# Kernel tuning notes

Measured on AMD Instinct MI355X. Metric: run time of the kernel, lower is better.

The kernel has to match this reference:

```python
import jax, jax.numpy as jnp
import numpy as np
from jax import lax

N_QUANTIZE = 256
N_AUX = 28
N_RESCH = 512
N_SKIPCH = 256
KS = 2
DILATIONS = [2 ** i for i in range(10)] * 3  # 30 layers
L = len(DILATIONS)


def _causal_conv(x, w, b, d):
    # x: (B, Cin, T), w: (Cout, Cin, KS) torch Conv1d layout, left-pad => causal
    pad = (w.shape[-1] - 1) * d
    y = lax.conv_general_dilated(x, w, window_strides=(1,), padding=[(pad, 0)],
                                 rhs_dilation=(d,),
                                 dimension_numbers=('NCH', 'OIH', 'NCH'))
    return y + b[None, :, None]


def _conv1x1(x, w, b):
    # x: (B, Cin, T), w: (Cout, Cin)
    return jnp.einsum('oi,bit->bot', w, x) + b[None, :, None]


def setup_inputs() -> dict:
    key = jax.random.key(0)
    ks = jax.random.split(key, 20)
    B, T = 2, 8000
    s = 0.05
    rn = lambda k, shape: (jax.random.normal(k, shape, jnp.float32) * s)
    inp = {
        'x': jax.random.randint(ks[0], (B, T), 0, N_QUANTIZE),
        'h': jax.random.normal(ks[1], (B, N_AUX, T), jnp.float32),
        'causal_w': rn(ks[2], (N_RESCH, N_QUANTIZE, KS)),
        'causal_b': rn(ks[3], (N_RESCH,)),
        'dil_sig_w': rn(ks[4], (L, N_RESCH, N_RESCH, KS)),
        'dil_sig_b': rn(ks[5], (L, N_RESCH)),
        'dil_tanh_w': rn(ks[6], (L, N_RESCH, N_RESCH, KS)),
        'dil_tanh_b': rn(ks[7], (L, N_RESCH)),
        'aux_sig_w': rn(ks[8], (L, N_RESCH, N_AUX)),
        'aux_sig_b': rn(ks[9], (L, N_RESCH)),
        'aux_tanh_w': rn(ks[10], (L, N_RESCH, N_AUX)),
        'aux_tanh_b': rn(ks[11], (L, N_RESCH)),
        'skip_w': rn(ks[12], (L, N_SKIPCH, N_RESCH)),
        'skip_b': rn(ks[13], (L, N_SKIPCH)),
        'res_w': rn(ks[14], (L, N_RESCH, N_RESCH)),
        'res_b': rn(ks[15], (L, N_RESCH)),
        'post1_w': rn(ks[16], (N_SKIPCH, N_SKIPCH)),
        'post1_b': rn(ks[17], (N_SKIPCH,)),
        'post2_w': rn(ks[18], (N_QUANTIZE, N_SKIPCH)),
        'post2_b': rn(ks[19], (N_QUANTIZE,)),
    }
    return inp


def reference(x, h, causal_w, causal_b, dil_sig_w, dil_sig_b, dil_tanh_w, dil_tanh_b,
              aux_sig_w, aux_sig_b, aux_tanh_w, aux_tanh_b, skip_w, skip_b,
              res_w, res_b, post1_w, post1_b, post2_w, post2_b):
    B, T = x.shape
    # _preprocess: onehot (B,T,Q) -> (B,Q,T), then causal conv
    oh = jax.nn.one_hot(x % N_QUANTIZE, N_QUANTIZE, dtype=jnp.float32).transpose(0, 2, 1)
    out = _causal_conv(oh, causal_w, causal_b, 1)  # (B, n_resch, T)
    skip_sum = jnp.zeros((B, N_SKIPCH, T), jnp.float32)
    for l, d in enumerate(DILATIONS):
        sig = _causal_conv(out, dil_sig_w[l], dil_sig_b[l], d) + _conv1x1(h, aux_sig_w[l], aux_sig_b[l])
        tan = _causal_conv(out, dil_tanh_w[l], dil_tanh_b[l], d) + _conv1x1(h, aux_tanh_w[l], aux_tanh_b[l])
        z = jax.nn.sigmoid(sig) * jnp.tanh(tan)
        skip_sum = skip_sum + _conv1x1(z, skip_w[l], skip_b[l])
        out = _conv1x1(z, res_w[l], res_b[l]) + out
    # _postprocess: relu -> 1x1 -> relu -> 1x1 -> (B, T, n_quantize)
    y = jax.nn.relu(skip_sum)
    y = jax.nn.relu(_conv1x1(y, post1_w, post1_b))
    y = _conv1x1(y, post2_w, post2_b)
    return y.transpose(0, 2, 1)
```

## Files before the change

### kernel.cpp

```cpp
#include <hip/hip_runtime.h>
#include <math.h>

#define T_LEN 8000
#define BATCH 2
#define CCH 512
#define SKP 256
#define AUXP 32
#define NQ 256
#define NLAYER 30
#define PADF 512
#define TPAD 8192
#define ROWS (PADF + TPAD)
#define HROWS TPAD

typedef unsigned short hfu;
typedef unsigned int u32;
typedef __attribute__((ext_vector_type(8))) _Float16 half8;
typedef __attribute__((ext_vector_type(4))) float f32x4;

#define GLOAD16(g, l)                                                          \
  __builtin_amdgcn_global_load_lds(                                            \
      (const __attribute__((address_space(1))) void*)(g),                      \
      (__attribute__((address_space(3))) void*)(l), 16, 0, 0)

__device__ inline hfu hfbits(float f) {
  union { _Float16 h; hfu u; } x;
  x.h = (_Float16)f;
  return x.u;
}
__device__ inline u32 pk2(float a, float b) {
  return (u32)hfbits(a) | ((u32)hfbits(b) << 16);
}
__device__ inline uint4 pk8(const float f[8]) {
  return make_uint4(pk2(f[0], f[1]), pk2(f[2], f[3]), pk2(f[4], f[5]), pk2(f[6], f[7]));
}
__device__ inline int ldsL(int row, int ck) {
  return ((row >> 1) << 3) + ((((ck) ^ ((row >> 1) & 3)) << 1) | (row & 1));
}

__global__ __launch_bounds__(256) void zero16(uint4* p, int n) {
  for (int i = blockIdx.x * 256 + threadIdx.x; i < n; i += gridDim.x * 256)
    p[i] = make_uint4(0u, 0u, 0u, 0u);
}

__global__ __launch_bounds__(256) void cvt_dil2(const float* __restrict__ inS,
                                                const float* __restrict__ inT,
                                                hfu* __restrict__ outS, hfu* __restrict__ outT) {
  const long NG = (long)NLAYER * CCH * (CCH / 4);
  for (long g2 = (long)blockIdx.x * 256 + threadIdx.x; g2 < 2 * NG; g2 += (long)gridDim.x * 256) {
    const int sel = (int)(g2 >= NG);
    const long g = sel ? (g2 - NG) : g2;
    const float* in = sel ? inT : inS;
    hfu* out = sel ? outT : outS;
    const int i4 = (int)(g & 127) * 4;
    const int o = (int)((g >> 7) & 511);
    const int l = (int)(g >> 16);
    const float* pp = in + (((size_t)l * CCH + o) * CCH + i4) * 2;
    float4 f0 = *(const float4*)pp;
    float4 f1 = *(const float4*)(pp + 4);
    uint2 t0 = make_uint2(pk2(f0.x, f0.z), pk2(f1.x, f1.z));
    uint2 t1 = make_uint2(pk2(f0.y, f0.w), pk2(f1.y, f1.w));
    hfu* ob = out + ((size_t)l * 2 * CCH + o) * CCH + i4;
    *(uint2*)ob = t0;
    *(uint2*)(ob + (size_t)CCH * CCH) = t1;
  }
}

__global__ __launch_bounds__(256) void cvt_skipres(const float* __restrict__ skw,
                                                   const float* __restrict__ rsw,
                                                   hfu* __restrict__ out) {
  const long NG = (long)NLAYER * 768 * (CCH / 4);
  for (long g = (long)blockIdx.x * 256 + threadIdx.x; g < NG; g += (long)gridDim.x * 256) {
    const int i4 = (int)(g & 127) * 4;
    const int r = (int)((g >> 7) % 768);
    const int l = (int)(g / (128 * 768));
    const float* src = (r < SKP) ? (skw + ((size_t)l * SKP + r) * CCH + i4)
                                 : (rsw + ((size_t)l * CCH + (r - SKP)) * CCH + i4);
    float4 f = *(const float4*)src;
    *(uint2*)(out + ((size_t)l * 768 + r) * CCH + i4) = make_uint2(pk2(f.x, f.y), pk2(f.z, f.w));
  }
}

__global__ __launch_bounds__(256) void cvt_aux(const float* __restrict__ in, hfu* __restrict__ out) {
  const int N = NLAYER * CCH * AUXP;
  for (int i = blockIdx.x * 256 + threadIdx.x; i < N; i += gridDim.x * 256) {
    const int j = i & 31;
    const int o = (i >> 5) & 511;
    const int l = i >> 14;
    float v = (j < 28) ? in[((size_t)l * CCH + o) * 28 + j] : 0.f;
    out[i] = hfbits(v);
  }
}

__global__ __launch_bounds__(256) void cvt_copy(const float* __restrict__ in, hfu* __restrict__ out, int n) {
  for (int i = blockIdx.x * 256 + threadIdx.x; i < n; i += gridDim.x * 256)
    out[i] = hfbits(in[i]);
}

__global__ __launch_bounds__(256) void cvt_cwt(const float* __restrict__ cw, float* __restrict__ out) {
  const int N = 2 * NQ * CCH;
  for (int i = blockIdx.x * 256 + threadIdx.x; i < N; i += gridDim.x * 256) {
    const int tap = i >> 17;
    const int r = i & 131071;
    const int xq = r >> 9;
    const int o = r & 511;
    out[i] = cw[((size_t)o * NQ + xq) * 2 + tap];
  }
}

__global__ __launch_bounds__(256) void htrans_kernel(const float* __restrict__ h, hfu* __restrict__ hbf) {
  const int b = blockIdx.y;
  const int t = blockIdx.x * 64 + (threadIdx.x & 63);
  const int j0 = threadIdx.x >> 6;
#pragma unroll
  for (int j = j0; j < AUXP; j += 4) {
    float v = (j < 28 && t < T_LEN) ? h[((size_t)b * 28 + j) * T_LEN + t] : 0.f;
    hbf[((size_t)b * HROWS + t) * AUXP + j] = hfbits(v);
  }
}

template <int PRE>
__global__ __launch_bounds__(256) void embed_kernel(const int* __restrict__ x,
                                                    const float* __restrict__ cwt,
                                                    const float* __restrict__ cb,
                                                    float* __restrict__ outf,
                                                    hfu* __restrict__ outb) {
  const int b = blockIdx.y;
  const int t = blockIdx.x * 4 + (threadIdx.x >> 6);
  const int o = (threadIdx.x & 63) * 8;
  const int xc = x[(size_t)b * T_LEN + t] & 255;
  const int xp = (t > 0) ? (x[(size_t)b * T_LEN + t - 1] & 255) : 0;
  const float won = (t > 0) ? 1.f : 0.f;
  const float* c1 = cwt + 131072 + (size_t)xc * CCH + o;
  const float* c0 = cwt + (size_t)xp * CCH + o;
  float v[8];
#pragma unroll
  for (int j = 0; j < 8; ++j) v[j] = cb[o + j] + c1[j] + won * c0[j];
  if (PRE) {
    *(uint4*)&outb[((size_t)b * ROWS + PADF + t) * CCH + o] = pk8(v);
  } else {
    float* po = outf + ((size_t)b * ROWS + PADF + t) * CCH + o;
    *(float4*)po = make_float4(v[0], v[1], v[2], v[3]);
    *(float4*)(po + 4) = make_float4(v[4], v[5], v[6], v[7]);
  }
}

template <int PRE>
__global__ __launch_bounds__(512, 2) void gate_kernel(
    const hfu* __restrict__ actb, const float* __restrict__ actf,
    const hfu* __restrict__ hbf,
    const void* __restrict__ wsp, const void* __restrict__ wtp,
    const hfu* __restrict__ auxs, const hfu* __restrict__ auxt,
    const float* __restrict__ bs1, const float* __restrict__ bs2,
    const float* __restrict__ bt1, const float* __restrict__ bt2,
    hfu* __restrict__ z, int d) {
  extern __shared__ uint4 smd[];
  const int tid = threadIdx.x;
  const int lane = tid & 63, wid = tid >> 6;
  const int wm = wid >> 2, wn = wid & 3;
  const int lr = lane & 15, lq = lane >> 4;

  const int n = blockIdx.x;
  const int f = (n & 7) * 32 + (n >> 3);
  const int tt = f >> 3, inner = f & 7;
  const int o0 = (inner >> 1) * 128;
  const int b = inner & 1;
  const int t0 = tt * 256;

  f32x4 accS[4][4] = {};
  f32x4 accT[4][4] = {};

  auto stage_dil = [&](int ih, int p) {
    const int base = p * 4096;
    const int tau = (ih < 8) ? 1 : 0;
    const int koff = (ih & 7) * 64;
    if (PRE) {
#pragma unroll
      for (int c = 0; c < 2; ++c) {
        const int s = c * 512 + tid;
        const int row = s >> 3, ck = (s & 7) ^ (row & 7);
        const size_t wo = ((size_t)tau * CCH + o0 + row) * CCH + koff + ck * 8;
        GLOAD16((const hfu*)wsp + wo, &smd[base + s]);
        GLOAD16((const hfu*)wtp + wo, &smd[base + 1024 + s]);
      }
#pragma unroll
      for (int c = 0; c < 4; ++c) {
        const int s = c * 512 + tid;
        const int row = s >> 3, ck = (s & 7) ^ (row & 7);
        const hfu* ar = actb + ((size_t)b * ROWS + PADF + t0 + row - (tau ? 0 : d)) * CCH + koff + ck * 8;
        GLOAD16(ar, &smd[base + 2048 + s]);
      }
    } else {
      const float* wsf = (const float*)wsp;
      const float* wtf = (const float*)wtp;
#pragma unroll
      for (int c = 0; c < 2; ++c) {
        const int s = c * 512 + tid;
        const int row = s >> 3, ck = (s & 7) ^ (row & 7);
        const size_t fb = ((size_t)(o0 + row) * CCH + koff + ck * 8) * 2;
        float vs[8], vt[8];
#pragma unroll
        for (int j = 0; j < 4; ++j) {
          float4 fs = *(const float4*)&wsf[fb + j * 4];
          float4 ft = *(const float4*)&wtf[fb + j * 4];
          vs[2 * j] = tau ? fs.y : fs.x;
          vs[2 * j + 1] = tau ? fs.w : fs.z;
          vt[2 * j] = tau ? ft.y : ft.x;
          vt[2 * j + 1] = tau ? ft.w : ft.z;
        }
        smd[base + s] = pk8(vs);
        smd[base + 1024 + s] = pk8(vt);
      }
#pragma unroll
      for (int c = 0; c < 4; ++c) {
        const int s = c * 512 + tid;
        const int row = s >> 3, ck = (s & 7) ^ (row & 7);
        const float* ar = actf + ((size_t)b * ROWS + PADF + t0 + row - (tau ? 0 : d)) * CCH + koff + ck * 8;
        float4 f0 = *(const float4*)&ar[0];
        float4 f1 = *(const float4*)&ar[4];
        float vb[8] = {f0.x, f0.y, f0.z, f0.w, f1.x, f1.y, f1.z, f1.w};
        smd[base + 2048 + s] = pk8(vb);
      }
    }
  };

  auto stage_aux = [&](int p) {
    const int base = p * 4096;
    {
      const int row = tid >> 2, ck = (tid & 3) ^ (row & 3);
      if (PRE) {
        GLOAD16(auxs + (size_t)(o0 + row) * AUXP + ck * 8, &smd[base + tid]);
        GLOAD16(auxt + (size_t)(o0 + row) * AUXP + ck * 8, &smd[base + 1024 + tid]);
      } else {
        smd[base + tid] = *(const uint4*)&auxs[(size_t)(o0 + row) * AUXP + ck * 8];
        smd[base + 1024 + tid] = *(const uint4*)&auxt[(size_t)(o0 + row) * AUXP + ck * 8];
      }
    }
#pragma unroll
    for (int c = 0; c < 2; ++c) {
      const int s = c * 512 + tid;
      const int row = s >> 2, ck = (s & 3) ^ (row & 3);
      if (PRE)
        GLOAD16(hbf + ((size_t)b * HROWS + t0 + row) * AUXP + ck * 8, &smd[base + 2048 + s]);
      else
        smd[base + 2048 + s] = *(const uint4*)&hbf[((size_t)b * HROWS + t0 + row) * AUXP + ck * 8];
    }
  };

  auto compute_dil = [&](int p) {
    const int base = p * 4096;
#pragma unroll
    for (int kk = 0; kk < 2; ++kk) {
      half8 af[4], ag[4], bv[4];
#pragma unroll
      for (int mr = 0; mr < 4; ++mr) {
        const int row = wm * 64 + mr * 16 + lr;
        const int idx = row * 8 + ((kk * 4 + lq) ^ (row & 7));
        af[mr] = *(const half8*)&smd[base + idx];
        ag[mr] = *(const half8*)&smd[base + 1024 + idx];
      }
#pragma unroll
      for (int nr = 0; nr < 4; ++nr) {
        const int row = wn * 64 + nr * 16 + lr;
        bv[nr] = *(const half8*)&smd[base + 2048 + row * 8 + ((kk * 4 + lq) ^ (row & 7))];
      }
#pragma unroll
      for (int mr = 0; mr < 4; ++mr)
#pragma unroll
        for (int nr = 0; nr < 4; ++nr) {
          accS[mr][nr] = __builtin_amdgcn_mfma_f32_16x16x32_f16(af[mr], bv[nr], accS[mr][nr], 0, 0, 0);
          accT[mr][nr] = __builtin_amdgcn_mfma_f32_16x16x32_f16(ag[mr], bv[nr], accT[mr][nr], 0, 0, 0);
        }
    }
  };

  auto compute_aux = [&](int p) {
    const int base = p * 4096;
    half8 af[4], ag[4], bv[4];
#pragma unroll
    for (int mr = 0; mr < 4; ++mr) {
      const int row = wm * 64 + mr * 16 + lr;
      const int idx = row * 4 + (lq ^ (row & 3));
      af[mr] = *(const half8*)&smd[base + idx];
      ag[mr] = *(const half8*)&smd[base + 1024 + idx];
    }
#pragma unroll
    for (int nr = 0; nr < 4; ++nr) {
      const int row = wn * 64 + nr * 16 + lr;
      bv[nr] = *(const half8*)&smd[base + 2048 + row * 4 + (lq ^ (row & 3))];
    }
#pragma unroll
    for (int mr = 0; mr < 4; ++mr)
#pragma unroll
      for (int nr = 0; nr < 4; ++nr) {
        accS[mr][nr] = __builtin_amdgcn_mfma_f32_16x16x32_f16(af[mr], bv[nr], accS[mr][nr], 0, 0, 0);
        accT[mr][nr] = __builtin_amdgcn_mfma_f32_16x16x32_f16(ag[mr], bv[nr], accT[mr][nr], 0, 0, 0);
      }
  };

  if (PRE) {
    stage_dil(0, 0);
    for (int ih = 0; ih < 17; ++ih) {
      if (ih < 15) {
        stage_dil(ih + 1, (ih + 1) & 1);
        asm volatile("s_waitcnt vmcnt(8)" ::: "memory");
      } else if (ih == 15) {
        stage_aux(0);
        asm volatile("s_waitcnt vmcnt(4)" ::: "memory");
      } else {
        asm volatile("s_waitcnt vmcnt(0)" ::: "memory");
      }
      __builtin_amdgcn_s_barrier();
      __builtin_amdgcn_sched_barrier(0);
      __builtin_amdgcn_s_setprio(1);
      if (ih < 16) compute_dil(ih & 1); else compute_aux(0);
      __builtin_amdgcn_s_setprio(0);
      __builtin_amdgcn_sched_barrier(0);
      __builtin_amdgcn_s_barrier();
    }
  } else {
    for (int ih = 0; ih < 17; ++ih) {
      if (ih < 16) stage_dil(ih, ih & 1); else stage_aux(0);
      __syncthreads();
      if (ih < 16) compute_dil(ih & 1); else compute_aux(0);
      __syncthreads();
    }
  }

#pragma unroll
  for (int mr = 0; mr < 4; ++mr) {
    const int ob = o0 + wm * 64 + mr * 16 + lq * 4;
    float4 x1 = *(const float4*)&bs1[ob];
    float4 x2 = *(const float4*)&bs2[ob];
    float4 y1 = *(const float4*)&bt1[ob];
    float4 y2 = *(const float4*)&bt2[ob];
    const float sb[4] = {x1.x + x2.x, x1.y + x2.y, x1.z + x2.z, x1.w + x2.w};
    const float tb[4] = {y1.x + y2.x, y1.y + y2.y, y1.z + y2.z, y1.w + y2.w};
#pragma unroll
    for (int nr = 0; nr < 4; ++nr) {
      const int t = t0 + wn * 64 + nr * 16 + lr;
      float zv[4];
#pragma unroll
      for (int j = 0; j < 4; ++j) {
        float sv = accS[mr][nr][j] + sb[j];
        float tv = accT[mr][nr][j] + tb[j];
        float sg = __builtin_amdgcn_rcpf(1.f + __expf(-sv));
        float e2 = __expf(2.f * tv);
        float th = 1.f - 2.f * __builtin_amdgcn_rcpf(e2 + 1.f);
        zv[j] = sg * th;
      }
      *(uint2*)&z[((size_t)b * HROWS + t) * CCH + ob] = make_uint2(pk2(zv[0], zv[1]), pk2(zv[2], zv[3]));
    }
  }
}

template <int PRE>
__global__ __launch_bounds__(512, 4) void update_kernel(
    const hfu* __restrict__ z, const void* __restrict__ wp,
    const float* __restrict__ skwf, const float* __restrict__ rswf,
    const float* __restrict__ skb, const float* __restrict__ rsb,
    float* __restrict__ skip, hfu* __restrict__ skiph,
    float* __restrict__ outf, hfu* __restrict__ outb) {
  __shared__ uint4 sm[2048];
  const int tid = threadIdx.x;
  const int lane = tid & 63, wid = tid >> 6;
  const int wm = wid >> 1, wn = wid & 1;
  const int lr = lane & 15, lq = lane >> 4;

  const int n = blockIdx.x;
  const int xcd = n & 7, j = n >> 3;
  const int ttl = j / 12, inner = j % 12;
  const int tt = xcd * 8 + ttl;
  if (tt > 62) return;
  const int rg = inner >> 1, b = inner & 1;
  const int r0 = rg * 128;
  const int t0 = tt * 128;

  f32x4 acc[2][4] = {};

  auto stage_u = [&](int ih, int p) {
    const int base = p * 1024;
    const int pr = tid >> 3, w = tid & 7;
    const int row = (pr << 1) | (w & 1);
    const int ck = (w >> 1) ^ (pr & 3);
    const int k0 = ih * 32;
    if (PRE) {
      GLOAD16((const hfu*)wp + (size_t)(r0 + row) * CCH + k0 + ck * 8, &sm[base + tid]);
      GLOAD16(z + ((size_t)b * HROWS + t0 + row) * CCH + k0 + ck * 8, &sm[base + 512 + tid]);
    } else {
      const int R = r0 + row;
      const float* src = (R < SKP) ? (skwf + (size_t)R * CCH + k0 + ck * 8)
                                   : (rswf + (size_t)(R - SKP) * CCH + k0 + ck * 8);
      float4 f0 = *(const float4*)&src[0];
      float4 f1 = *(const float4*)&src[4];
      float v[8] = {f0.x, f0.y, f0.z, f0.w, f1.x, f1.y, f1.z, f1.w};
      sm[base + tid] = pk8(v);
      sm[base + 512 + tid] = *(const uint4*)&z[((size_t)b * HROWS + t0 + row) * CCH + k0 + ck * 8];
    }
  };

  auto compute_u = [&](int p) {
    const int base = p * 1024;
    half8 av[2], bv[4];
#pragma unroll
    for (int mr = 0; mr < 2; ++mr) {
      const int row = wm * 32 + mr * 16 + lr;
      av[mr] = *(const half8*)&sm[base + ldsL(row, lq)];
    }
#pragma unroll
    for (int nr = 0; nr < 4; ++nr) {
      const int row = wn * 64 + nr * 16 + lr;
      bv[nr] = *(const half8*)&sm[base + 512 + ldsL(row, lq)];
    }
#pragma unroll
    for (int mr = 0; mr < 2; ++mr)
#pragma unroll
      for (int nr = 0; nr < 4; ++nr)
        acc[mr][nr] = __builtin_amdgcn_mfma_f32_16x16x32_f16(av[mr], bv[nr], acc[mr][nr], 0, 0, 0);
  };

  if (PRE) {
    stage_u(0, 0);
    for (int ih = 0; ih < 16; ++ih) {
      if (ih < 15) {
        stage_u(ih + 1, (ih + 1) & 1);
        asm volatile("s_waitcnt vmcnt(2)" ::: "memory");
      } else {
        asm volatile("s_waitcnt vmcnt(0)" ::: "memory");
      }
      __builtin_amdgcn_s_barrier();
      __builtin_amdgcn_sched_barrier(0);
      __builtin_amdgcn_s_setprio(1);
      compute_u(ih & 1);
      __builtin_amdgcn_s_setprio(0);
      __builtin_amdgcn_sched_barrier(0);
      __builtin_amdgcn_s_barrier();
    }
  } else {
    for (int ih = 0; ih < 16; ++ih) {
      stage_u(ih, ih & 1);
      __syncthreads();
      compute_u(ih & 1);
      __syncthreads();
    }
  }

  const bool iskip = (r0 < SKP);
#pragma unroll
  for (int mr = 0; mr < 2; ++mr) {
    const int R = r0 + wm * 32 + mr * 16 + lq * 4;
#pragma unroll
    for (int nr = 0; nr < 4; ++nr) {
      const int t = t0 + wn * 64 + nr * 16 + lr;
      if (t < T_LEN) {
        if (iskip) {
          float4 bb = *(const float4*)&skb[R];
          if (PRE) {
            hfu* ps = &skiph[((size_t)b * T_LEN + t) * SKP + R];
            uint2 old = *(uint2*)ps;
            const _Float16* hp = (const _Float16*)&old;
            float v0 = (float)hp[0] + acc[mr][nr][0] + bb.x;
            float v1 = (float)hp[1] + acc[mr][nr][1] + bb.y;
            float v2 = (float)hp[2] + acc[mr][nr][2] + bb.z;
            float v3 = (float)hp[3] + acc[mr][nr][3] + bb.w;
            *(uint2*)ps = make_uint2(pk2(v0, v1), pk2(v2, v3));
          } else {
            float4* p = (float4*)&skip[((size_t)b * T_LEN + t) * SKP + R];
            float4 v = *p;
            v.x += acc[mr][nr][0] + bb.x;
            v.y += acc[mr][nr][1] + bb.y;
            v.z += acc[mr][nr][2] + bb.z;
            v.w += acc[mr][nr][3] + bb.w;
            *p = v;
          }
        } else {
          const int rr = R - SKP;
          float4 bb = *(const float4*)&rsb[rr];
          if (PRE) {
            hfu* pb = &outb[((size_t)b * ROWS + PADF + t) * CCH + rr];
            uint2 old = *(uint2*)pb;
            const _Float16* hp = (const _Float16*)&old;
            float v0 = (float)hp[0] + acc[mr][nr][0] + bb.x;
            float v1 = (float)hp[1] + acc[mr][nr][1] + bb.y;
            float v2 = (float)hp[2] + acc[mr][nr][2] + bb.z;
            float v3 = (float)hp[3] + acc[mr][nr][3] + bb.w;
            *(uint2*)pb = make_uint2(pk2(v0, v1), pk2(v2, v3));
          } else {
            float4* p = (float4*)&outf[((size_t)b * ROWS + PADF + t) * CCH + rr];
            float4 v = *p;
            v.x += acc[mr][nr][0] + bb.x;
            v.y += acc[mr][nr][1] + bb.y;
            v.z += acc[mr][nr][2] + bb.z;
            v.w += acc[mr][nr][3] + bb.w;
            *p = v;
          }
        }
      }
    }
  }
}

template <int PRE>
__global__ __launch_bounds__(256, 2) void post1_kernel(const float* __restrict__ skip,
                                                       const hfu* __restrict__ skiph,
                                                       const hfu* __restrict__ w,
                                                       const float* __restrict__ bias,
                                                       hfu* __restrict__ y1) {
  __shared__ uint4 sm[2048];
  uint4* sA = sm;
  uint4* sB = sm + 1024;
  const int tid = threadIdx.x;
  const int lane = tid & 63, wid = tid >> 6;
  const int wm = wid >> 1, wn = wid & 1;
  const int lr = lane & 15, lq = lane >> 4;
  const int t0 = blockIdx.x * 128;
  const int r0 = blockIdx.y * 128;
  const int b = blockIdx.z;
  f32x4 acc[4][4] = {};
  for (int kt = 0; kt < 4; ++kt) {
#pragma unroll
    for (int c = 0; c < 4; ++c) {
      const int cb = c * 256 + wid * 64;
      const int ch = cb + lane;
      const int ksub = ch >> 7, mn = ch & 127;
      const int k0 = kt * 64 + ksub * 8;
      GLOAD16(w + (size_t)(r0 + mn) * SKP + k0, &sA[cb]);
      int row = t0 + mn;
      if (row > T_LEN - 1) row = T_LEN - 1;
      if (PRE) {
        uint4 u = *(const uint4*)&skiph[((size_t)b * T_LEN + row) * SKP + k0];
        const _Float16* hp = (const _Float16*)&u;
        float v[8];
#pragma unroll
        for (int j = 0; j < 8; ++j) v[j] = fmaxf((float)hp[j], 0.f);
        sB[ch] = pk8(v);
      } else {
        const float* src = skip + ((size_t)b * T_LEN + row) * SKP + k0;
        float4 f0 = *(const float4*)&src[0];
        float4 f1 = *(const float4*)&src[4];
        float v[8] = {fmaxf(f0.x, 0.f), fmaxf(f0.y, 0.f), fmaxf(f0.z, 0.f), fmaxf(f0.w, 0.f),
                      fmaxf(f1.x, 0.f), fmaxf(f1.y, 0.f), fmaxf(f1.z, 0.f), fmaxf(f1.w, 0.f)};
        sB[ch] = pk8(v);
      }
    }
    __syncthreads();
#pragma unroll
    for (int ks = 0; ks < 2; ++ks) {
      const int kb = (ks * 4 + lq) * 128;
      half8 av[4], bv[4];
#pragma unroll
      for (int r = 0; r < 4; ++r) {
        av[r] = *(const half8*)&sA[kb + wm * 64 + r * 16 + lr];
        bv[r] = *(const half8*)&sB[kb + wn * 64 + r * 16 + lr];
      }
#pragma unroll
      for (int mr = 0; mr < 4; ++mr)
#pragma unroll
        for (int nr = 0; nr < 4; ++nr)
          acc[mr][nr] = __builtin_amdgcn_mfma_f32_16x16x32_f16(av[mr], bv[nr], acc[mr][nr], 0, 0, 0);
    }
    __syncthreads();
  }
#pragma unroll
  for (int mr = 0; mr < 4; ++mr) {
    const int ob = r0 + wm * 64 + mr * 16 + lq * 4;
    float4 bb = *(const float4*)&bias[ob];
    const float bs[4] = {bb.x, bb.y, bb.z, bb.w};
#pragma unroll
    for (int nr = 0; nr < 4; ++nr) {
      const int t = t0 + wn * 64 + nr * 16 + lr;
      float v[4];
#pragma unroll
      for (int j = 0; j < 4; ++j) v[j] = fmaxf(acc[mr][nr][j] + bs[j], 0.f);
      *(uint2*)&y1[((size_t)b * HROWS + t) * SKP + ob] = make_uint2(pk2(v[0], v[1]), pk2(v[2], v[3]));
    }
  }
}

__global__ __launch_bounds__(256, 2) void post2_kernel(const hfu* __restrict__ y1,
                                                       const hfu* __restrict__ w,
                                                       const float* __restrict__ bias,
                                                       float* __restrict__ outp) {
  __shared__ uint4 sm[2048];
  uint4* sA = sm;
  uint4* sB = sm + 1024;
  const int tid = threadIdx.x;
  const int lane = tid & 63, wid = tid >> 6;
  const int wm = wid >> 1, wn = wid & 1;
  const int lr = lane & 15, lq = lane >> 4;
  const int t0 = blockIdx.x * 128;
  const int r0 = blockIdx.y * 128;
  const int b = blockIdx.z;
  f32x4 acc[4][4] = {};
  for (int kt = 0; kt < 4; ++kt) {
#pragma unroll
    for (int c = 0; c < 4; ++c) {
      const int cb = c * 256 + wid * 64;
      const int ch = cb + lane;
      const int ksub = ch >> 7, mn = ch & 127;
      const int k0 = kt * 64 + ksub * 8;
      GLOAD16(w + (size_t)(r0 + mn) * SKP + k0, &sA[cb]);
      GLOAD16(y1 + ((size_t)b * HROWS + t0 + mn) * SKP + k0, &sB[cb]);
    }
    __syncthreads();
#pragma unroll
    for (int ks = 0; ks < 2; ++ks) {
      const int kb = (ks * 4 + lq) * 128;
      half8 av[4], bv[4];
#pragma unroll
      for (int r = 0; r < 4; ++r) {
        av[r] = *(const half8*)&sA[kb + wm * 64 + r * 16 + lr];
        bv[r] = *(const half8*)&sB[kb + wn * 64 + r * 16 + lr];
      }
#pragma unroll
      for (int mr = 0; mr < 4; ++mr)
#pragma unroll
        for (int nr = 0; nr < 4; ++nr)
          acc[mr][nr] = __builtin_amdgcn_mfma_f32_16x16x32_f16(av[mr], bv[nr], acc[mr][nr], 0, 0, 0);
    }
    __syncthreads();
  }
#pragma unroll
  for (int mr = 0; mr < 4; ++mr) {
    const int ob = r0 + wm * 64 + mr * 16 + lq * 4;
    float4 bb = *(const float4*)&bias[ob];
#pragma unroll
    for (int nr = 0; nr < 4; ++nr) {
      const int t = t0 + wn * 64 + nr * 16 + lr;
      if (t < T_LEN) {
        float4 v;
        v.x = acc[mr][nr][0] + bb.x;
        v.y = acc[mr][nr][1] + bb.y;
        v.z = acc[mr][nr][2] + bb.z;
        v.w = acc[mr][nr][3] + bb.w;
        *(float4*)&outp[((size_t)b * T_LEN + t) * NQ + ob] = v;
      }
    }
  }
}

extern "C" void kernel_launch(void* const* d_in, const int* in_sizes, int n_in,
                              void* d_out, int out_size, void* d_ws, size_t ws_size,
                              hipStream_t stream) {
  const int* x = (const int*)d_in[0];
  const float* h = (const float*)d_in[1];
  const float* causal_w = (const float*)d_in[2];
  const float* causal_b = (const float*)d_in[3];
  const float* dil_sig_w = (const float*)d_in[4];
  const float* dil_sig_b = (const float*)d_in[5];
  const float* dil_tanh_w = (const float*)d_in[6];
  const float* dil_tanh_b = (const float*)d_in[7];
  const float* aux_sig_w = (const float*)d_in[8];
  const float* aux_sig_b = (const float*)d_in[9];
  const float* aux_tanh_w = (const float*)d_in[10];
  const float* aux_tanh_b = (const float*)d_in[11];
  const float* skip_w = (const float*)d_in[12];
  const float* skip_b = (const float*)d_in[13];
  const float* res_w = (const float*)d_in[14];
  const float* res_b = (const float*)d_in[15];
  const float* post1_w = (const float*)d_in[16];
  const float* post1_b = (const float*)d_in[17];
  const float* post2_w = (const float*)d_in[18];
  const float* post2_b = (const float*)d_in[19];
  float* outp = (float*)d_out;

  hipFuncSetAttribute((const void*)gate_kernel<1>,
                      hipFuncAttributeMaxDynamicSharedMemorySize, 131072);
  hipFuncSetAttribute((const void*)gate_kernel<0>,
                      hipFuncAttributeMaxDynamicSharedMemorySize, 131072);

  char* p = (char*)d_ws;
  auto alloc = [&](size_t bytes) {
    char* r = p;
    p += (bytes + 255) & ~(size_t)255;
    return r;
  };
  float* outf = (float*)alloc((size_t)BATCH * ROWS * CCH * 4);
  float* skip = (float*)alloc((size_t)BATCH * T_LEN * SKP * 4);
  hfu* zb = (hfu*)alloc((size_t)BATCH * HROWS * CCH * 2);
  hfu* hbf = (hfu*)alloc((size_t)BATCH * HROWS * AUXP * 2);
  hfu* auxsb = (hfu*)alloc((size_t)NLAYER * CCH * AUXP * 2);
  hfu* auxtb = (hfu*)alloc((size_t)NLAYER * CCH * AUXP * 2);
  hfu* p1b = (hfu*)alloc((size_t)NQ * SKP * 2);
  hfu* p2b = (hfu*)alloc((size_t)NQ * SKP * 2);
  float* cwt = (float*)alloc((size_t)2 * NQ * CCH * 4);
  hfu* skiph = (hfu*)alloc((size_t)BATCH * T_LEN * SKP * 2);
  hfu* y1 = zb;
  hfu* outb = (hfu*)alloc((size_t)BATCH * ROWS * CCH * 2);
  hfu* dilS = (hfu*)alloc((size_t)NLAYER * 2 * CCH * CCH * 2);
  hfu* dilT = (hfu*)alloc((size_t)NLAYER * 2 * CCH * CCH * 2);
  hfu* wsr = (hfu*)alloc((size_t)NLAYER * 768 * CCH * 2);
  const bool pre = ((size_t)(p - (char*)d_ws) <= ws_size);

  cvt_aux<<<256, 256, 0, stream>>>(aux_sig_w, auxsb);
  cvt_aux<<<256, 256, 0, stream>>>(aux_tanh_w, auxtb);
  cvt_copy<<<64, 256, 0, stream>>>(post1_w, p1b, NQ * SKP);
  cvt_copy<<<64, 256, 0, stream>>>(post2_w, p2b, NQ * SKP);
  cvt_cwt<<<1024, 256, 0, stream>>>(causal_w, cwt);
  if (pre) {
    cvt_dil2<<<4096, 256, 0, stream>>>(dil_sig_w, dil_tanh_w, dilS, dilT);
    cvt_skipres<<<2048, 256, 0, stream>>>(skip_w, res_w, wsr);
  }

  if (pre) {
    zero16<<<512, 256, 0, stream>>>((uint4*)skiph, (int)((size_t)BATCH * T_LEN * SKP * 2 / 16));
    for (int b = 0; b < BATCH; ++b) {
      zero16<<<32, 256, 0, stream>>>((uint4*)(outb + (size_t)b * ROWS * CCH), PADF * CCH * 2 / 16);
      zero16<<<48, 256, 0, stream>>>((uint4*)(outb + ((size_t)b * ROWS + PADF + T_LEN) * CCH),
                                     (TPAD - T_LEN) * CCH * 2 / 16);
    }
  } else {
    zero16<<<512, 256, 0, stream>>>((uint4*)skip, (int)((size_t)BATCH * T_LEN * SKP * 4 / 16));
    for (int b = 0; b < BATCH; ++b) {
      zero16<<<64, 256, 0, stream>>>((uint4*)(outf + (size_t)b * ROWS * CCH), PADF * CCH * 4 / 16);
      zero16<<<96, 256, 0, stream>>>((uint4*)(outf + ((size_t)b * ROWS + PADF + T_LEN) * CCH),
                                     (TPAD - T_LEN) * CCH * 4 / 16);
    }
  }

  htrans_kernel<<<dim3(128, 2), 256, 0, stream>>>(h, hbf);
  if (pre)
    embed_kernel<1><<<dim3(2000, 2), 256, 0, stream>>>(x, cwt, causal_b, nullptr, outb);
  else
    embed_kernel<0><<<dim3(2000, 2), 256, 0, stream>>>(x, cwt, causal_b, outf, nullptr);

  for (int l = 0; l < NLAYER; ++l) {
    const int d = 1 << (l % 10);
    if (pre) {
      gate_kernel<1><<<256, 512, 131072, stream>>>(
          outb, nullptr, hbf, dilS + (size_t)l * 2 * CCH * CCH, dilT + (size_t)l * 2 * CCH * CCH,
          auxsb + (size_t)l * CCH * AUXP, auxtb + (size_t)l * CCH * AUXP,
          dil_sig_b + (size_t)l * CCH, aux_sig_b + (size_t)l * CCH,
          dil_tanh_b + (size_t)l * CCH, aux_tanh_b + (size_t)l * CCH, zb, d);
      update_kernel<1><<<768, 512, 0, stream>>>(
          zb, wsr + (size_t)l * 768 * CCH, nullptr, nullptr,
          skip_b + (size_t)l * SKP, res_b + (size_t)l * CCH, nullptr, skiph, nullptr, outb);
    } else {
      gate_kernel<0><<<256, 512, 131072, stream>>>(
          nullptr, outf, hbf, dil_sig_w + (size_t)l * CCH * CCH * 2,
          dil_tanh_w + (size_t)l * CCH * CCH * 2,
          auxsb + (size_t)l * CCH * AUXP, auxtb + (size_t)l * CCH * AUXP,
          dil_sig_b + (size_t)l * CCH, aux_sig_b + (size_t)l * CCH,
          dil_tanh_b + (size_t)l * CCH, aux_tanh_b + (size_t)l * CCH, zb, d);
      update_kernel<0><<<768, 512, 0, stream>>>(
          zb, nullptr, skip_w + (size_t)l * SKP * CCH, res_w + (size_t)l * CCH * CCH,
          skip_b + (size_t)l * SKP, res_b + (size_t)l * CCH, skip, nullptr, outf, nullptr);
    }
  }

  if (pre)
    post1_kernel<1><<<dim3(63, 2, BATCH), 256, 0, stream>>>(nullptr, skiph, p1b, post1_b, y1);
  else
    post1_kernel<0><<<dim3(63, 2, BATCH), 256, 0, stream>>>(skip, nullptr, p1b, post1_b, y1);
  post2_kernel<<<dim3(63, 2, BATCH), 256, 0, stream>>>(y1, p2b, post2_b, outp);
}
```

Before: 2.087 ms.

## Restructure dilated and skip/res GEMM pipelines with precomputed pointers and single barrier

Rewrites the PRE path of the dilated-conv GEMM and the skip/res GEMM main loops. They now wait for the current stage, read its first fragments from LDS, then issue the next stage's global-to-LDS loads before the MFMAs run. Each iteration uses one barrier instead of two, and global pointers and LDS offsets are computed once and advanced incrementally, cutting address arithmetic and sync cost. The weight conversion kernel also switches to 8-element vectors per thread with 16-byte stores. The tradeoff is a wait on vmcnt(0) at the top of every iteration, so load/compute overlap now depends on the load landing within one compute phase.

```diff
diff --git a/kernel.cpp b/kernel.cpp
--- a/kernel.cpp
+++ b/kernel.cpp
@@ -43,26 +43,28 @@
     p[i] = make_uint4(0u, 0u, 0u, 0u);
 }
 
-__global__ __launch_bounds__(256) void cvt_dil2(const float* __restrict__ inS,
-                                                const float* __restrict__ inT,
-                                                hfu* __restrict__ outS, hfu* __restrict__ outT) {
-  const long NG = (long)NLAYER * CCH * (CCH / 4);
+__global__ __launch_bounds__(256) void cvt_dil2b(const float* __restrict__ inS,
+                                                 const float* __restrict__ inT,
+                                                 hfu* __restrict__ outS, hfu* __restrict__ outT) {
+  const long NG = (long)NLAYER * CCH * (CCH / 8);
   for (long g2 = (long)blockIdx.x * 256 + threadIdx.x; g2 < 2 * NG; g2 += (long)gridDim.x * 256) {
     const int sel = (int)(g2 >= NG);
     const long g = sel ? (g2 - NG) : g2;
     const float* in = sel ? inT : inS;
     hfu* out = sel ? outT : outS;
-    const int i4 = (int)(g & 127) * 4;
-    const int o = (int)((g >> 7) & 511);
-    const int l = (int)(g >> 16);
-    const float* pp = in + (((size_t)l * CCH + o) * CCH + i4) * 2;
-    float4 f0 = *(const float4*)pp;
-    float4 f1 = *(const float4*)(pp + 4);
-    uint2 t0 = make_uint2(pk2(f0.x, f0.z), pk2(f1.x, f1.z));
-    uint2 t1 = make_uint2(pk2(f0.y, f0.w), pk2(f1.y, f1.w));
-    hfu* ob = out + ((size_t)l * 2 * CCH + o) * CCH + i4;
-    *(uint2*)ob = t0;
-    *(uint2*)(ob + (size_t)CCH * CCH) = t1;
+    const int i8 = (int)(g & 63) * 8;
+    const int o = (int)((g >> 6) & 511);
+    const int l = (int)(g >> 15);
+    const float* pp = in + (((size_t)l * CCH + o) * CCH + i8) * 2;
+    float4 a = *(const float4*)pp;
+    float4 bq = *(const float4*)(pp + 4);
+    float4 c = *(const float4*)(pp + 8);
+    float4 e = *(const float4*)(pp + 12);
+    const float t0[8] = {a.x, a.z, bq.x, bq.z, c.x, c.z, e.x, e.z};
+    const float t1[8] = {a.y, a.w, bq.y, bq.w, c.y, c.w, e.y, e.w};
+    hfu* ob = out + ((size_t)l * 2 * CCH + o) * CCH + i8;
+    *(uint4*)ob = pk8(t0);
+    *(uint4*)(ob + (size_t)CCH * CCH) = pk8(t1);
   }
 }
 
@@ -170,27 +172,155 @@
   f32x4 accS[4][4] = {};
   f32x4 accT[4][4] = {};
 
-  auto stage_dil = [&](int ih, int p) {
-    const int base = p * 4096;
-    const int tau = (ih < 8) ? 1 : 0;
-    const int koff = (ih & 7) * 64;
-    if (PRE) {
-#pragma unroll
-      for (int c = 0; c < 2; ++c) {
-        const int s = c * 512 + tid;
-        const int row = s >> 3, ck = (s & 7) ^ (row & 7);
-        const size_t wo = ((size_t)tau * CCH + o0 + row) * CCH + koff + ck * 8;
-        GLOAD16((const hfu*)wsp + wo, &smd[base + s]);
-        GLOAD16((const hfu*)wtp + wo, &smd[base + 1024 + s]);
-      }
-#pragma unroll
-      for (int c = 0; c < 4; ++c) {
-        const int s = c * 512 + tid;
-        const int row = s >> 3, ck = (s & 7) ^ (row & 7);
-        const hfu* ar = actb + ((size_t)b * ROWS + PADF + t0 + row - (tau ? 0 : d)) * CCH + koff + ck * 8;
-        GLOAD16(ar, &smd[base + 2048 + s]);
-      }
-    } else {
+  if (PRE) {
+    const int sw0 = tid, sw1 = 512 + tid;
+    const int rw0 = sw0 >> 3, cw0 = (sw0 & 7) ^ (rw0 & 7);
+    const int rw1 = sw1 >> 3, cw1 = (sw1 & 7) ^ (rw1 & 7);
+    const hfu* wsP0 = (const hfu*)wsp + ((size_t)CCH + o0 + rw0) * CCH + cw0 * 8;
+    const hfu* wsP1 = (const hfu*)wsp + ((size_t)CCH + o0 + rw1) * CCH + cw1 * 8;
+    const hfu* wtP0 = (const hfu*)wtp + ((size_t)CCH + o0 + rw0) * CCH + cw0 * 8;
+    const hfu* wtP1 = (const hfu*)wtp + ((size_t)CCH + o0 + rw1) * CCH + cw1 * 8;
+    const hfu *a1P0, *a1P1, *a1P2, *a1P3, *a0P0, *a0P1, *a0P2, *a0P3;
+    {
+      const int s0 = tid, s1 = 512 + tid, s2 = 1024 + tid, s3 = 1536 + tid;
+      const int r0_ = s0 >> 3, c0_ = (s0 & 7) ^ (r0_ & 7);
+      const int r1_ = s1 >> 3, c1_ = (s1 & 7) ^ (r1_ & 7);
+      const int r2_ = s2 >> 3, c2_ = (s2 & 7) ^ (r2_ & 7);
+      const int r3_ = s3 >> 3, c3_ = (s3 & 7) ^ (r3_ & 7);
+      const hfu* base1 = actb + ((size_t)b * ROWS + PADF + t0) * CCH;
+      a1P0 = base1 + (size_t)r0_ * CCH + c0_ * 8;
+      a1P1 = base1 + (size_t)r1_ * CCH + c1_ * 8;
+      a1P2 = base1 + (size_t)r2_ * CCH + c2_ * 8;
+      a1P3 = base1 + (size_t)r3_ * CCH + c3_ * 8;
+      const hfu* base0 = actb + ((size_t)b * ROWS + PADF + t0 - d) * CCH;
+      a0P0 = base0 + (size_t)r0_ * CCH + c0_ * 8;
+      a0P1 = base0 + (size_t)r1_ * CCH + c1_ * 8;
+      a0P2 = base0 + (size_t)r2_ * CCH + c2_ * 8;
+      a0P3 = base0 + (size_t)r3_ * CCH + c3_ * 8;
+    }
+    int offA[2][4], offB[2][4];
+#pragma unroll
+    for (int kk = 0; kk < 2; ++kk) {
+#pragma unroll
+      for (int mr = 0; mr < 4; ++mr) {
+        const int row = wm * 64 + mr * 16 + lr;
+        offA[kk][mr] = row * 8 + ((kk * 4 + lq) ^ (row & 7));
+      }
+#pragma unroll
+      for (int nr = 0; nr < 4; ++nr) {
+        const int row = wn * 64 + nr * 16 + lr;
+        offB[kk][nr] = row * 8 + ((kk * 4 + lq) ^ (row & 7));
+      }
+    }
+
+    auto issue_stage = [&](int ihs) {
+      uint4* dst = smd + ((ihs & 1) << 12);
+      if (ihs < 16) {
+        GLOAD16(wsP0, &dst[tid]);
+        GLOAD16(wsP1, &dst[512 + tid]);
+        GLOAD16(wtP0, &dst[1024 + tid]);
+        GLOAD16(wtP1, &dst[1536 + tid]);
+        if (ihs < 8) {
+          GLOAD16(a1P0, &dst[2048 + tid]);
+          GLOAD16(a1P1, &dst[2560 + tid]);
+          GLOAD16(a1P2, &dst[3072 + tid]);
+          GLOAD16(a1P3, &dst[3584 + tid]);
+          a1P0 += 64; a1P1 += 64; a1P2 += 64; a1P3 += 64;
+        } else {
+          GLOAD16(a0P0, &dst[2048 + tid]);
+          GLOAD16(a0P1, &dst[2560 + tid]);
+          GLOAD16(a0P2, &dst[3072 + tid]);
+          GLOAD16(a0P3, &dst[3584 + tid]);
+          a0P0 += 64; a0P1 += 64; a0P2 += 64; a0P3 += 64;
+        }
+        if (ihs == 7) {
+          wsP0 -= 262592; wsP1 -= 262592; wtP0 -= 262592; wtP1 -= 262592;
+        } else {
+          wsP0 += 64; wsP1 += 64; wtP0 += 64; wtP1 += 64;
+        }
+      } else {
+        {
+          const int row = tid >> 2, ck = (tid & 3) ^ (row & 3);
+          GLOAD16(auxs + (size_t)(o0 + row) * AUXP + ck * 8, &dst[tid]);
+          GLOAD16(auxt + (size_t)(o0 + row) * AUXP + ck * 8, &dst[1024 + tid]);
+        }
+#pragma unroll
+        for (int c = 0; c < 2; ++c) {
+          const int s = c * 512 + tid;
+          const int row = s >> 2, ck = (s & 3) ^ (row & 3);
+          GLOAD16(hbf + ((size_t)b * HROWS + t0 + row) * AUXP + ck * 8, &dst[2048 + s]);
+        }
+      }
+    };
+
+    issue_stage(0);
+    for (int ih = 0; ih < 17; ++ih) {
+      asm volatile("s_waitcnt vmcnt(0)" ::: "memory");
+      __builtin_amdgcn_s_barrier();
+      __builtin_amdgcn_sched_barrier(0);
+      const uint4* base = smd + ((ih & 1) << 12);
+      if (ih < 16) {
+        half8 af[4], ag[4], bv[4];
+#pragma unroll
+        for (int mr = 0; mr < 4; ++mr) {
+          af[mr] = *(const half8*)&base[offA[0][mr]];
+          ag[mr] = *(const half8*)&base[1024 + offA[0][mr]];
+        }
+#pragma unroll
+        for (int nr = 0; nr < 4; ++nr) bv[nr] = *(const half8*)&base[2048 + offB[0][nr]];
+        issue_stage(ih + 1);
+        __builtin_amdgcn_s_setprio(1);
+#pragma unroll
+        for (int mr = 0; mr < 4; ++mr)
+#pragma unroll
+          for (int nr = 0; nr < 4; ++nr) {
+            accS[mr][nr] = __builtin_amdgcn_mfma_f32_16x16x32_f16(af[mr], bv[nr], accS[mr][nr], 0, 0, 0);
+            accT[mr][nr] = __builtin_amdgcn_mfma_f32_16x16x32_f16(ag[mr], bv[nr], accT[mr][nr], 0, 0, 0);
+          }
+#pragma unroll
+        for (int mr = 0; mr < 4; ++mr) {
+          af[mr] = *(const half8*)&base[offA[1][mr]];
+          ag[mr] = *(const half8*)&base[1024 + offA[1][mr]];
+        }
+#pragma unroll
+        for (int nr = 0; nr < 4; ++nr) bv[nr] = *(const half8*)&base[2048 + offB[1][nr]];
+#pragma unroll
+        for (int mr = 0; mr < 4; ++mr)
+#pragma unroll
+          for (int nr = 0; nr < 4; ++nr) {
+            accS[mr][nr] = __builtin_amdgcn_mfma_f32_16x16x32_f16(af[mr], bv[nr], accS[mr][nr], 0, 0, 0);
+            accT[mr][nr] = __builtin_amdgcn_mfma_f32_16x16x32_f16(ag[mr], bv[nr], accT[mr][nr], 0, 0, 0);
+          }
+        __builtin_amdgcn_s_setprio(0);
+        __builtin_amdgcn_sched_barrier(0);
+      } else {
+        half8 af[4], ag[4], bv[4];
+#pragma unroll
+        for (int mr = 0; mr < 4; ++mr) {
+          const int row = wm * 64 + mr * 16 + lr;
+          const int idx = row * 4 + (lq ^ (row & 3));
+          af[mr] = *(const half8*)&base[idx];
+          ag[mr] = *(const half8*)&base[1024 + idx];
+        }
+#pragma unroll
+        for (int nr = 0; nr < 4; ++nr) {
+          const int row = wn * 64 + nr * 16 + lr;
+          bv[nr] = *(const half8*)&base[2048 + row * 4 + (lq ^ (row & 3))];
+        }
+#pragma unroll
+        for (int mr = 0; mr < 4; ++mr)
+#pragma unroll
+          for (int nr = 0; nr < 4; ++nr) {
+            accS[mr][nr] = __builtin_amdgcn_mfma_f32_16x16x32_f16(af[mr], bv[nr], accS[mr][nr], 0, 0, 0);
+            accT[mr][nr] = __builtin_amdgcn_mfma_f32_16x16x32_f16(ag[mr], bv[nr], accT[mr][nr], 0, 0, 0);
+          }
+      }
+    }
+  } else {
+    auto stage_dil = [&](int ih, int p) {
+      const int base = p * 4096;
+      const int tau = (ih < 8) ? 1 : 0;
+      const int koff = (ih & 7) * 64;
       const float* wsf = (const float*)wsp;
       const float* wtf = (const float*)wtp;
 #pragma unroll
@@ -221,108 +351,71 @@
         float vb[8] = {f0.x, f0.y, f0.z, f0.w, f1.x, f1.y, f1.z, f1.w};
         smd[base + 2048 + s] = pk8(vb);
       }
-    }
-  };
-
-  auto stage_aux = [&](int p) {
-    const int base = p * 4096;
-    {
-      const int row = tid >> 2, ck = (tid & 3) ^ (row & 3);
-      if (PRE) {
-        GLOAD16(auxs + (size_t)(o0 + row) * AUXP + ck * 8, &smd[base + tid]);
-        GLOAD16(auxt + (size_t)(o0 + row) * AUXP + ck * 8, &smd[base + 1024 + tid]);
-      } else {
+    };
+    auto stage_aux0 = [&](int p) {
+      const int base = p * 4096;
+      {
+        const int row = tid >> 2, ck = (tid & 3) ^ (row & 3);
         smd[base + tid] = *(const uint4*)&auxs[(size_t)(o0 + row) * AUXP + ck * 8];
         smd[base + 1024 + tid] = *(const uint4*)&auxt[(size_t)(o0 + row) * AUXP + ck * 8];
       }
-    }
-#pragma unroll
-    for (int c = 0; c < 2; ++c) {
-      const int s = c * 512 + tid;
-      const int row = s >> 2, ck = (s & 3) ^ (row & 3);
-      if (PRE)
-        GLOAD16(hbf + ((size_t)b * HROWS + t0 + row) * AUXP + ck * 8, &smd[base + 2048 + s]);
-      else
+#pragma unroll
+      for (int c = 0; c < 2; ++c) {
+        const int s = c * 512 + tid;
+        const int row = s >> 2, ck = (s & 3) ^ (row & 3);
         smd[base + 2048 + s] = *(const uint4*)&hbf[((size_t)b * HROWS + t0 + row) * AUXP + ck * 8];
-    }
-  };
-
-  auto compute_dil = [&](int p) {
-    const int base = p * 4096;
-#pragma unroll
-    for (int kk = 0; kk < 2; ++kk) {
-      half8 af[4], ag[4], bv[4];
-#pragma unroll
-      for (int mr = 0; mr < 4; ++mr) {
-        const int row = wm * 64 + mr * 16 + lr;
-        const int idx = row * 8 + ((kk * 4 + lq) ^ (row & 7));
-        af[mr] = *(const half8*)&smd[base + idx];
-        ag[mr] = *(const half8*)&smd[base + 1024 + idx];
-      }
-#pragma unroll
-      for (int nr = 0; nr < 4; ++nr) {
-        const int row = wn * 64 + nr * 16 + lr;
-        bv[nr] = *(const half8*)&smd[base + 2048 + row * 8 + ((kk * 4 + lq) ^ (row & 7))];
-      }
-#pragma unroll
-      for (int mr = 0; mr < 4; ++mr)
+      }
+    };
+    for (int ih = 0; ih < 17; ++ih) {
+      if (ih < 16) stage_dil(ih, ih & 1); else stage_aux0(0);
+      __syncthreads();
+      const uint4* base = smd + ((ih & 1) << 12);
+      if (ih < 16) {
+#pragma unroll
+        for (int kk = 0; kk < 2; ++kk) {
+          half8 af[4], ag[4], bv[4];
+#pragma unroll
+          for (int mr = 0; mr < 4; ++mr) {
+            const int row = wm * 64 + mr * 16 + lr;
+            const int idx = row * 8 + ((kk * 4 + lq) ^ (row & 7));
+            af[mr] = *(const half8*)&base[idx];
+            ag[mr] = *(const half8*)&base[1024 + idx];
+          }
+#pragma unroll
+          for (int nr = 0; nr < 4; ++nr) {
+            const int row = wn * 64 + nr * 16 + lr;
+            bv[nr] = *(const half8*)&base[2048 + row * 8 + ((kk * 4 + lq) ^ (row & 7))];
+          }
+#pragma unroll
+          for (int mr = 0; mr < 4; ++mr)
+#pragma unroll
+            for (int nr = 0; nr < 4; ++nr) {
+              accS[mr][nr] = __builtin_amdgcn_mfma_f32_16x16x32_f16(af[mr], bv[nr], accS[mr][nr], 0, 0, 0);
+              accT[mr][nr] = __builtin_amdgcn_mfma_f32_16x16x32_f16(ag[mr], bv[nr], accT[mr][nr], 0, 0, 0);
+            }
+        }
+      } else {
+        half8 af[4], ag[4], bv[4];
+#pragma unroll
+        for (int mr = 0; mr < 4; ++mr) {
+          const int row = wm * 64 + mr * 16 + lr;
+          const int idx = row * 4 + (lq ^ (row & 3));
+          af[mr] = *(const half8*)&base[idx];
+          ag[mr] = *(const half8*)&base[1024 + idx];
+        }
 #pragma unroll
         for (int nr = 0; nr < 4; ++nr) {
-          accS[mr][nr] = __builtin_amdgcn_mfma_f32_16x16x32_f16(af[mr], bv[nr], accS[mr][nr], 0, 0, 0);
-          accT[mr][nr] = __builtin_amdgcn_mfma_f32_16x16x32_f16(ag[mr], bv[nr], accT[mr][nr], 0, 0, 0);
-        }
-    }
-  };
-
-  auto compute_aux = [&](int p) {
-    const int base = p * 4096;
-    half8 af[4], ag[4], bv[4];
-#pragma unroll
-    for (int mr = 0; mr < 4; ++mr) {
-      const int row = wm * 64 + mr * 16 + lr;
-      const int idx = row * 4 + (lq ^ (row & 3));
-      af[mr] = *(const half8*)&smd[base + idx];
-      ag[mr] = *(const half8*)&smd[base + 1024 + idx];
-    }
-#pragma unroll
-    for (int nr = 0; nr < 4; ++nr) {
-      const int row = wn * 64 + nr * 16 + lr;
-      bv[nr] = *(const half8*)&smd[base + 2048 + row * 4 + (lq ^ (row & 3))];
-    }
-#pragma unroll
-    for (int mr = 0; mr < 4; ++mr)
-#pragma unroll
-      for (int nr = 0; nr < 4; ++nr) {
-        accS[mr][nr] = __builtin_amdgcn_mfma_f32_16x16x32_f16(af[mr], bv[nr], accS[mr][nr], 0, 0, 0);
-        accT[mr][nr] = __builtin_amdgcn_mfma_f32_16x16x32_f16(ag[mr], bv[nr], accT[mr][nr], 0, 0, 0);
-      }
-  };
-
-  if (PRE) {
-    stage_dil(0, 0);
-    for (int ih = 0; ih < 17; ++ih) {
-      if (ih < 15) {
-        stage_dil(ih + 1, (ih + 1) & 1);
-        asm volatile("s_waitcnt vmcnt(8)" ::: "memory");
-      } else if (ih == 15) {
-        stage_aux(0);
-        asm volatile("s_waitcnt vmcnt(4)" ::: "memory");
-      } else {
-        asm volatile("s_waitcnt vmcnt(0)" ::: "memory");
-      }
-      __builtin_amdgcn_s_barrier();
-      __builtin_amdgcn_sched_barrier(0);
-      __builtin_amdgcn_s_setprio(1);
-      if (ih < 16) compute_dil(ih & 1); else compute_aux(0);
-      __builtin_amdgcn_s_setprio(0);
-      __builtin_amdgcn_sched_barrier(0);
-      __builtin_amdgcn_s_barrier();
-    }
-  } else {
-    for (int ih = 0; ih < 17; ++ih) {
-      if (ih < 16) stage_dil(ih, ih & 1); else stage_aux(0);
-      __syncthreads();
-      if (ih < 16) compute_dil(ih & 1); else compute_aux(0);
+          const int row = wn * 64 + nr * 16 + lr;
+          bv[nr] = *(const half8*)&base[2048 + row * 4 + (lq ^ (row & 3))];
+        }
+#pragma unroll
+        for (int mr = 0; mr < 4; ++mr)
+#pragma unroll
+          for (int nr = 0; nr < 4; ++nr) {
+            accS[mr][nr] = __builtin_amdgcn_mfma_f32_16x16x32_f16(af[mr], bv[nr], accS[mr][nr], 0, 0, 0);
+            accT[mr][nr] = __builtin_amdgcn_mfma_f32_16x16x32_f16(ag[mr], bv[nr], accT[mr][nr], 0, 0, 0);
+          }
+      }
       __syncthreads();
     }
   }
@@ -377,17 +470,51 @@
   const int t0 = tt * 128;
 
   f32x4 acc[2][4] = {};
-
-  auto stage_u = [&](int ih, int p) {
-    const int base = p * 1024;
-    const int pr = tid >> 3, w = tid & 7;
-    const int row = (pr << 1) | (w & 1);
-    const int ck = (w >> 1) ^ (pr & 3);
-    const int k0 = ih * 32;
-    if (PRE) {
-      GLOAD16((const hfu*)wp + (size_t)(r0 + row) * CCH + k0 + ck * 8, &sm[base + tid]);
-      GLOAD16(z + ((size_t)b * HROWS + t0 + row) * CCH + k0 + ck * 8, &sm[base + 512 + tid]);
-    } else {
+  const int pr = tid >> 3, w = tid & 7;
+  const int row = (pr << 1) | (w & 1);
+  const int ck = (w >> 1) ^ (pr & 3);
+
+  if (PRE) {
+    const hfu* wPtr = (const hfu*)wp + (size_t)(r0 + row) * CCH + ck * 8;
+    const hfu* zPtr = z + ((size_t)b * HROWS + t0 + row) * CCH + ck * 8;
+    int offa[2], offb[4];
+#pragma unroll
+    for (int mr = 0; mr < 2; ++mr) offa[mr] = ldsL(wm * 32 + mr * 16 + lr, lq);
+#pragma unroll
+    for (int nr = 0; nr < 4; ++nr) offb[nr] = ldsL(wn * 64 + nr * 16 + lr, lq);
+
+    GLOAD16(wPtr, &sm[tid]);
+    GLOAD16(zPtr, &sm[512 + tid]);
+    wPtr += 32; zPtr += 32;
+    for (int ih = 0; ih < 16; ++ih) {
+      asm volatile("s_waitcnt vmcnt(0)" ::: "memory");
+      __builtin_amdgcn_s_barrier();
+      __builtin_amdgcn_sched_barrier(0);
+      const uint4* base = sm + ((ih & 1) << 10);
+      half8 av[2], bv[4];
+#pragma unroll
+      for (int mr = 0; mr < 2; ++mr) av[mr] = *(const half8*)&base[offa[mr]];
+#pragma unroll
+      for (int nr = 0; nr < 4; ++nr) bv[nr] = *(const half8*)&base[512 + offb[nr]];
+      if (ih < 15) {
+        uint4* dst = sm + (((ih + 1) & 1) << 10);
+        GLOAD16(wPtr, &dst[tid]);
+        GLOAD16(zPtr, &dst[512 + tid]);
+        wPtr += 32; zPtr += 32;
+      }
+      __builtin_amdgcn_s_setprio(1);
+#pragma unroll
+      for (int mr = 0; mr < 2; ++mr)
+#pragma unroll
+        for (int nr = 0; nr < 4; ++nr)
+          acc[mr][nr] = __builtin_amdgcn_mfma_f32_16x16x32_f16(av[mr], bv[nr], acc[mr][nr], 0, 0, 0);
+      __builtin_amdgcn_s_setprio(0);
+      __builtin_amdgcn_sched_barrier(0);
+    }
+  } else {
+    for (int ih = 0; ih < 16; ++ih) {
+      const int base = (ih & 1) * 1024;
+      const int k0 = ih * 32;
       const int R = r0 + row;
       const float* src = (R < SKP) ? (skwf + (size_t)R * CCH + k0 + ck * 8)
                                    : (rswf + (size_t)(R - SKP) * CCH + k0 + ck * 8);
@@ -396,51 +523,17 @@
       float v[8] = {f0.x, f0.y, f0.z, f0.w, f1.x, f1.y, f1.z, f1.w};
       sm[base + tid] = pk8(v);
       sm[base + 512 + tid] = *(const uint4*)&z[((size_t)b * HROWS + t0 + row) * CCH + k0 + ck * 8];
-    }
-  };
-
-  auto compute_u = [&](int p) {
-    const int base = p * 1024;
-    half8 av[2], bv[4];
-#pragma unroll
-    for (int mr = 0; mr < 2; ++mr) {
-      const int row = wm * 32 + mr * 16 + lr;
-      av[mr] = *(const half8*)&sm[base + ldsL(row, lq)];
-    }
-#pragma unroll
-    for (int nr = 0; nr < 4; ++nr) {
-      const int row = wn * 64 + nr * 16 + lr;
-      bv[nr] = *(const half8*)&sm[base + 512 + ldsL(row, lq)];
-    }
-#pragma unroll
-    for (int mr = 0; mr < 2; ++mr)
-#pragma unroll
-      for (int nr = 0; nr < 4; ++nr)
-        acc[mr][nr] = __builtin_amdgcn_mfma_f32_16x16x32_f16(av[mr], bv[nr], acc[mr][nr], 0, 0, 0);
-  };
-
-  if (PRE) {
-    stage_u(0, 0);
-    for (int ih = 0; ih < 16; ++ih) {
-      if (ih < 15) {
-        stage_u(ih + 1, (ih + 1) & 1);
-        asm volatile("s_waitcnt vmcnt(2)" ::: "memory");
-      } else {
-        asm volatile("s_waitcnt vmcnt(0)" ::: "memory");
-      }
-      __builtin_amdgcn_s_barrier();
-      __builtin_amdgcn_sched_barrier(0);
-      __builtin_amdgcn_s_setprio(1);
-      compute_u(ih & 1);
-      __builtin_amdgcn_s_setprio(0);
-      __builtin_amdgcn_sched_barrier(0);
-      __builtin_amdgcn_s_barrier();
-    }
-  } else {
-    for (int ih = 0; ih < 16; ++ih) {
-      stage_u(ih, ih & 1);
       __syncthreads();
-      compute_u(ih & 1);
+      half8 av[2], bv[4];
+#pragma unroll
+      for (int mr = 0; mr < 2; ++mr) av[mr] = *(const half8*)&sm[base + ldsL(wm * 32 + mr * 16 + lr, lq)];
+#pragma unroll
+      for (int nr = 0; nr < 4; ++nr) bv[nr] = *(const half8*)&sm[base + 512 + ldsL(wn * 64 + nr * 16 + lr, lq)];
+#pragma unroll
+      for (int mr = 0; mr < 2; ++mr)
+#pragma unroll
+        for (int nr = 0; nr < 4; ++nr)
+          acc[mr][nr] = __builtin_amdgcn_mfma_f32_16x16x32_f16(av[mr], bv[nr], acc[mr][nr], 0, 0, 0);
       __syncthreads();
     }
   }
@@ -532,7 +625,7 @@
         const _Float16* hp = (const _Float16*)&u;
         float v[8];
 #pragma unroll
-        for (int j = 0; j < 8; ++j) v[j] = fmaxf((float)hp[j], 0.f);
+        for (int jj = 0; jj < 8; ++jj) v[jj] = fmaxf((float)hp[jj], 0.f);
         sB[ch] = pk8(v);
       } else {
         const float* src = skip + ((size_t)b * T_LEN + row) * SKP + k0;
@@ -571,7 +664,7 @@
       const int t = t0 + wn * 64 + nr * 16 + lr;
       float v[4];
 #pragma unroll
-      for (int j = 0; j < 4; ++j) v[j] = fmaxf(acc[mr][nr][j] + bs[j], 0.f);
+      for (int jj = 0; jj < 4; ++jj) v[jj] = fmaxf(acc[mr][nr][jj] + bs[jj], 0.f);
       *(uint2*)&y1[((size_t)b * HROWS + t) * SKP + ob] = make_uint2(pk2(v[0], v[1]), pk2(v[2], v[3]));
     }
   }
@@ -698,7 +791,7 @@
   cvt_copy<<<64, 256, 0, stream>>>(post2_w, p2b, NQ * SKP);
   cvt_cwt<<<1024, 256, 0, stream>>>(causal_w, cwt);
   if (pre) {
-    cvt_dil2<<<4096, 256, 0, stream>>>(dil_sig_w, dil_tanh_w, dilS, dilT);
+    cvt_dil2b<<<2048, 256, 0, stream>>>(dil_sig_w, dil_tanh_w, dilS, dilT);
     cvt_skipres<<<2048, 256, 0, stream>>>(skip_w, res_w, wsr);
   }
 
```

Result: faster. 2.027 ms (median of 2 runs) (-2.9%).
